# Kernel optimization log

Measured on AMD Instinct MI355X. Metric: run time of the kernel, lower is better.

Reference implementation:

```python
import jax, jax.numpy as jnp
import numpy as np

N_HEAD = 16
N_EMBD = 64  # per-head dim in this module's convention
INNER = N_HEAD * N_EMBD  # 1024


def setup_inputs() -> dict:
    key = jax.random.key(0)
    ks = jax.random.split(key, 6)
    B, S = 4, 2048
    scale = 0.02
    return {
        "x": jax.random.normal(ks[0], (B, S, N_EMBD), dtype=jnp.float32),
        "Wq": jax.random.normal(ks[1], (N_EMBD, INNER), dtype=jnp.float32) * scale,
        "Wk": jax.random.normal(ks[2], (N_EMBD, INNER), dtype=jnp.float32) * scale,
        "Wv": jax.random.normal(ks[3], (N_EMBD, INNER), dtype=jnp.float32) * scale,
        "Wo": jax.random.normal(ks[4], (INNER, N_EMBD), dtype=jnp.float32) * scale,
        "bo": jax.random.normal(ks[5], (N_EMBD,), dtype=jnp.float32) * scale,
        "causal_mask": 1,
    }


def reference(x, Wq, Wk, Wv, Wo, bo, causal_mask):
    B, S, _ = x.shape
    # projections: [B,S,INNER] -> [B,H,S,D]
    def split_heads(t):
        return t.reshape(B, S, N_HEAD, N_EMBD).transpose(0, 2, 1, 3)
    q = split_heads(x @ Wq)
    k = split_heads(x @ Wk)
    v = split_heads(x @ Wv)
    # [B,H,S,S]
    scores = jnp.einsum("bhqd,bhkd->bhqk", q, k) / jnp.sqrt(jnp.float32(N_EMBD))
    if causal_mask:
        future = jnp.triu(jnp.ones((S, S), dtype=scores.dtype), k=1)
        scores = scores - 1e9 * future  # matches torch: subtract 1e9*mask
    attn = jax.nn.softmax(scores, axis=-1)
    out = jnp.einsum("bhqk,bhkd->bhqd", attn, v)
    out = out.transpose(0, 2, 1, 3).reshape(B, S, INNER)
    return out @ Wo + bo
```

## Files before the change

kernel.cpp:

```cpp
#include <hip/hip_runtime.h>
#include <hip/hip_bf16.h>

#define NHEAD 16
#define HDIM 64
#define DINNER 1024
#define NBATCH 4
#define SEQ 2048
#define NTOK (NBATCH*SEQ)

typedef __bf16 bf16;
typedef __bf16 bf16x2 __attribute__((ext_vector_type(2)));
typedef __bf16 bf16x4 __attribute__((ext_vector_type(4)));
typedef __bf16 bf16x8 __attribute__((ext_vector_type(8)));
typedef float f32x4 __attribute__((ext_vector_type(4)));
typedef float f32x16 __attribute__((ext_vector_type(16)));
typedef unsigned int u32;
typedef unsigned int u32x2 __attribute__((ext_vector_type(2)));
typedef unsigned int u32x4 __attribute__((ext_vector_type(4)));

#define OFF_BO   8
#define OFF_XB   128
#define OFF_WQT  (OFF_XB + NTOK*HDIM)
#define OFF_WKT  (OFF_WQT + DINNER*HDIM)
#define OFF_WVT  (OFF_WKT + DINNER*HDIM)
#define OFF_WOT  (OFF_WVT + DINNER*HDIM)
#define OFF_Q    (OFF_WOT + DINNER*HDIM)
#define OFF_K    (OFF_Q + NTOK*DINNER)
#define OFF_VT   (OFF_K + NTOK*DINNER)
#define OFF_ATT  (OFF_VT + NTOK*DINNER)
#define OFF_ATT2 (OFF_ATT + NTOK*DINNER)
#define OFF_L    (OFF_ATT2 + NTOK*DINNER)

#define SSCALE 0.18033688011112042f

static __device__ __forceinline__ bf16x8 ld8(const bf16* p) {
  return *reinterpret_cast<const bf16x8*>(p);
}

static __device__ __forceinline__ u32 pkbf(float a, float b) {
  bf16x2 t; t[0] = (bf16)a; t[1] = (bf16)b;
  return __builtin_bit_cast(u32, t);
}

static __device__ __forceinline__ int detect_isbf(const void* x, int tid,
                                                  int* sflag) {
  if (tid < 64) {
    const unsigned short* xb = (const unsigned short*)x;
    bool ok = true;
#pragma unroll
    for (int i = 0; i < 8; i++) {
      unsigned e = (xb[tid * 8 + i] >> 7) & 0xFF;
      ok = ok && (e >= 64 && e <= 140);
    }
    unsigned long long mball = __ballot(ok);
    if (tid == 0) *sflag = (mball == ~0ull) ? 1 : 0;
  }
  __syncthreads();
  return *sflag;
}

__global__ __launch_bounds__(256) void prep_kernel(
    const void* __restrict__ x, const void* __restrict__ Wq,
    const void* __restrict__ Wk, const void* __restrict__ Wv,
    const void* __restrict__ Wo, const void* __restrict__ bo,
    bf16* __restrict__ ws) {
  __shared__ int sflag;
  int isbf = detect_isbf(x, threadIdx.x, &sflag);
  int z = blockIdx.y;
  int idx = blockIdx.x * 256 + threadIdx.x;
  if (z < 3) {
    const void* src = (z == 0) ? Wq : (z == 1) ? Wk : Wv;
    bf16* dst = ws + ((z == 0) ? OFF_WQT : (z == 1) ? OFF_WKT : OFF_WVT);
    int d = idx >> 10, n = idx & 1023;
    float v = isbf ? (float)((const bf16*)src)[idx] : ((const float*)src)[idx];
    if (z == 0) v *= SSCALE;
    dst[n * HDIM + d] = (bf16)v;
  } else if (z == 3) {
    int k = idx >> 6, n = idx & 63;
    float v = isbf ? (float)((const bf16*)Wo)[idx] : ((const float*)Wo)[idx];
    ws[OFF_WOT + n * DINNER + k] = (bf16)v;
  } else if (z == 4) {
    int i = idx * 8;
    bf16x8 v;
    if (isbf) {
      v = ld8((const bf16*)x + i);
    } else {
      f32x4 a = *reinterpret_cast<const f32x4*>((const float*)x + i);
      f32x4 b2 = *reinterpret_cast<const f32x4*>((const float*)x + i + 4);
#pragma unroll
      for (int j = 0; j < 4; j++) { v[j] = (bf16)a[j]; v[4 + j] = (bf16)b2[j]; }
    }
    *reinterpret_cast<bf16x8*>(&ws[OFF_XB + i]) = v;
  } else {
    if (idx < 64) ws[OFF_BO + idx] = isbf ? ((const bf16*)bo)[idx] : (bf16)((const float*)bo)[idx];
  }
}

__global__ __launch_bounds__(256) void qkv_kernel(bf16* __restrict__ ws) {
  __shared__ __align__(16) bf16 Vst[4][16 * 72];
  int tt = blockIdx.x, pz = blockIdx.z;
  int w = threadIdx.x >> 6;
  int nc = blockIdx.y * 4 + w;
  int lane = threadIdx.x & 63;
  int lq = lane & 15, quad = lane >> 4;
  const bf16* WT = ws + OFF_WQT + pz * (DINNER * HDIM);
  int n0 = nc * 64;
  bf16x8 w0[4], w1[4];
#pragma unroll
  for (int c = 0; c < 4; c++) {
    const bf16* wr = WT + (n0 + c * 16 + lq) * HDIM;
    w0[c] = ld8(wr + quad * 8);
    w1[c] = ld8(wr + 32 + quad * 8);
  }
  bf16* Qb = ws + OFF_Q;
  bf16* Kb = ws + OFF_K;
  bf16* VTb = ws + OFF_VT;
  bf16x8 ao0[4], ao1[4];
  if (pz == 2) {
    const bf16* WoT = ws + OFF_WOT;
#pragma unroll
    for (int c = 0; c < 4; c++) {
      const bf16* orow = WoT + (size_t)(c * 16 + lq) * DINNER + nc * 64;
      ao0[c] = ld8(orow + quad * 8);
      ao1[c] = ld8(orow + 32 + quad * 8);
    }
  }
#pragma unroll
  for (int mi = 0; mi < 4; mi++) {
    int t0 = tt * 64 + mi * 16;
    const bf16* xrow = ws + OFF_XB + (t0 + lq) * HDIM;
    bf16x8 x0 = ld8(xrow + quad * 8);
    bf16x8 x1 = ld8(xrow + 32 + quad * 8);
    int b = t0 >> 11, s0 = t0 & (SEQ - 1);
    if (pz < 2) {
#pragma unroll
      for (int c = 0; c < 4; c++) {
        f32x4 z = {0.f, 0.f, 0.f, 0.f};
        z = __builtin_amdgcn_mfma_f32_16x16x32_bf16(w0[c], x0, z, 0, 0, 0);
        z = __builtin_amdgcn_mfma_f32_16x16x32_bf16(w1[c], x1, z, 0, 0, 0);
        bf16x4 pk = {(bf16)z[0], (bf16)z[1], (bf16)z[2], (bf16)z[3]};
        bf16* P = (pz == 0) ? Qb : Kb;
        *reinterpret_cast<bf16x4*>(
            &P[((size_t)(b * NHEAD + nc) * SEQ + s0 + lq) * HDIM + c * 16 + quad * 4]) = pk;
      }
    } else {
#pragma unroll
      for (int c = 0; c < 4; c++) {
        f32x4 z = {0.f, 0.f, 0.f, 0.f};
        z = __builtin_amdgcn_mfma_f32_16x16x32_bf16(w0[c], x0, z, 0, 0, 0);
        z = __builtin_amdgcn_mfma_f32_16x16x32_bf16(w1[c], x1, z, 0, 0, 0);
        bf16x4 pk = {(bf16)z[0], (bf16)z[1], (bf16)z[2], (bf16)z[3]};
        *reinterpret_cast<bf16x4*>(&Vst[w][lq * 72 + c * 16 + quad * 4]) = pk;
      }
      bf16x8 bv0 = ld8(&Vst[w][lq * 72 + quad * 8]);
      bf16x8 bv1 = ld8(&Vst[w][lq * 72 + 32 + quad * 8]);
#pragma unroll
      for (int c = 0; c < 4; c++) {
        f32x4 z2 = {0.f, 0.f, 0.f, 0.f};
        z2 = __builtin_amdgcn_mfma_f32_16x16x32_bf16(ao0[c], bv0, z2, 0, 0, 0);
        z2 = __builtin_amdgcn_mfma_f32_16x16x32_bf16(ao1[c], bv1, z2, 0, 0, 0);
#pragma unroll
        for (int r = 0; r < 4; r++) {
          int d = c * 16 + quad * 4 + r;
          VTb[(((size_t)b * NHEAD + nc) * HDIM + d) * SEQ + s0 + lq] = (bf16)z2[r];
        }
      }
    }
  }
}

__global__ __launch_bounds__(256, 2) void flash_kernel(const int* __restrict__ cmask,
                                                       bf16* __restrict__ ws) {
  __shared__ __align__(16) bf16 Kl[2][64 * 64];
  __shared__ __align__(16) bf16 Vl[2][64 * 64];
  int bid = blockIdx.x;
  int bh = (bid & 7) * 8 + ((bid >> 3) & 7);
  int z = (bid >> 6) & 7;
  int half = bid >> 9;
  int w = threadIdx.x >> 6;
  int lane = threadIdx.x & 63;
  int ql = lane & 31, lh = lane >> 5, l7 = lane & 7;
  int causal = cmask[0];
  const bf16* Q = ws + OFF_Q + (size_t)bh * SEQ * HDIM;
  const bf16* K = ws + OFF_K + (size_t)bh * SEQ * HDIM;
  const bf16* VT = ws + OFF_VT + (size_t)bh * HDIM * SEQ;
  int b = bh >> 4, h = bh & 15;
  bf16* ar = ws + OFF_ATT + (size_t)half * NTOK * DINNER;
  float* Lp = reinterpret_cast<float*>(ws + OFF_L) + (size_t)half * NTOK * NHEAD;
  int sr = threadIdx.x >> 2;
  int sg = (threadIdx.x & 3) * 16;
  int sc0 = (((threadIdx.x & 3) * 2) ^ (sr & 7)) << 3;
  int sc1 = (((threadIdx.x & 3) * 2 + 1) ^ (sr & 7)) << 3;

  int bufc = 0;

  for (int seg = 0; seg < 2; ++seg) {
    int qt = seg ? (15 - z) : z;
    int Ts = causal ? (seg ? (32 - 2 * z) : (2 * z + 2)) : 32;
    int hs = Ts >> 1;
    int t0 = half * hs, t1 = t0 + hs;
    int qb = qt * 128;
    int qw = qb + w * 32;
    int qa = qw + ql;

    bf16x8 bq[4];
#pragma unroll
    for (int dsub = 0; dsub < 4; dsub++)
      bq[dsub] = ld8(Q + (size_t)qa * HDIM + dsub * 16 + lh * 8);

    f32x16 o0, o1;
#pragma unroll
    for (int r = 0; r < 16; r++) { o0[r] = 0.f; o1[r] = 0.f; }
    float lsum = 0.f;

    bf16x8 kst0 = ld8(K + (size_t)(t0 * 64 + sr) * HDIM + sg);
    bf16x8 kst1 = ld8(K + (size_t)(t0 * 64 + sr) * HDIM + sg + 8);
    bf16x8 vst0 = ld8(VT + (size_t)sr * SEQ + t0 * 64 + sg);
    bf16x8 vst1 = ld8(VT + (size_t)sr * SEQ + t0 * 64 + sg + 8);

    for (int ti = t0; ti < t1; ++ti, ++bufc) {
      int buf = bufc & 1;
      int k0 = ti * 64;
      *reinterpret_cast<bf16x8*>(&Kl[buf][sr * 64 + sc0]) = kst0;
      *reinterpret_cast<bf16x8*>(&Kl[buf][sr * 64 + sc1]) = kst1;
      *reinterpret_cast<bf16x8*>(&Vl[buf][sr * 64 + sc0]) = vst0;
      *reinterpret_cast<bf16x8*>(&Vl[buf][sr * 64 + sc1]) = vst1;
      int kn = (ti + 1 < t1) ? (k0 + 64) : k0;
      kst0 = ld8(K + (size_t)(kn + sr) * HDIM + sg);
      kst1 = ld8(K + (size_t)(kn + sr) * HDIM + sg + 8);
      vst0 = ld8(VT + (size_t)sr * SEQ + kn + sg);
      vst1 = ld8(VT + (size_t)sr * SEQ + kn + sg + 8);
      __syncthreads();
      if (causal && k0 > qw + 31) continue;

      f32x16 s0, s1;
#pragma unroll
      for (int r = 0; r < 16; r++) { s0[r] = 0.f; s1[r] = 0.f; }
      __builtin_amdgcn_s_setprio(1);
#pragma unroll
      for (int dsub = 0; dsub < 4; dsub++) {
        int co = ((dsub * 2 + lh) ^ l7) << 3;
        bf16x8 a0 = ld8(&Kl[buf][ql * 64 + co]);
        bf16x8 a1 = ld8(&Kl[buf][(32 + ql) * 64 + co]);
        s0 = __builtin_amdgcn_mfma_f32_32x32x16_bf16(a0, bq[dsub], s0, 0, 0, 0);
        s1 = __builtin_amdgcn_mfma_f32_32x32x16_bf16(a1, bq[dsub], s1, 0, 0, 0);
      }
      __builtin_amdgcn_s_setprio(0);

      if (causal && (k0 + 63 > qw)) {
#pragma unroll
        for (int r = 0; r < 16; r++) {
          int kk = k0 + (r & 3) + 8 * (r >> 2) + 4 * lh;
          if (kk > qa) s0[r] = -200.0f;
          if (kk + 32 > qa) s1[r] = -200.0f;
        }
      }

      bf16x8 pf[4];
      {
        float e[16];
#pragma unroll
        for (int r = 0; r < 16; r++) { e[r] = exp2f(s0[r]); lsum += e[r]; }
#pragma unroll
        for (int j = 0; j < 2; j++) {
          u32 x0 = pkbf(e[8 * j + 0], e[8 * j + 1]);
          u32 x1 = pkbf(e[8 * j + 2], e[8 * j + 3]);
          u32 y0 = pkbf(e[8 * j + 4], e[8 * j + 5]);
          u32 y1 = pkbf(e[8 * j + 6], e[8 * j + 7]);
          u32x2 r0 = __builtin_amdgcn_permlane32_swap(x0, y0, false, false);
          u32x2 r1 = __builtin_amdgcn_permlane32_swap(x1, y1, false, false);
          u32x4 fw = {r0[0], r1[0], r0[1], r1[1]};
          pf[j] = __builtin_bit_cast(bf16x8, fw);
        }
      }
      {
        float e[16];
#pragma unroll
        for (int r = 0; r < 16; r++) { e[r] = exp2f(s1[r]); lsum += e[r]; }
#pragma unroll
        for (int j = 0; j < 2; j++) {
          u32 x0 = pkbf(e[8 * j + 0], e[8 * j + 1]);
          u32 x1 = pkbf(e[8 * j + 2], e[8 * j + 3]);
          u32 y0 = pkbf(e[8 * j + 4], e[8 * j + 5]);
          u32 y1 = pkbf(e[8 * j + 6], e[8 * j + 7]);
          u32x2 r0 = __builtin_amdgcn_permlane32_swap(x0, y0, false, false);
          u32x2 r1 = __builtin_amdgcn_permlane32_swap(x1, y1, false, false);
          u32x4 fw = {r0[0], r1[0], r0[1], r1[1]};
          pf[2 + j] = __builtin_bit_cast(bf16x8, fw);
        }
      }

      __builtin_amdgcn_s_setprio(1);
#pragma unroll
      for (int ks = 0; ks < 4; ks++) {
        int co = ((ks * 2 + lh) ^ l7) << 3;
        bf16x8 av0 = ld8(&Vl[buf][ql * 64 + co]);
        bf16x8 av1 = ld8(&Vl[buf][(32 + ql) * 64 + co]);
        o0 = __builtin_amdgcn_mfma_f32_32x32x16_bf16(av0, pf[ks], o0, 0, 0, 0);
        o1 = __builtin_amdgcn_mfma_f32_32x32x16_bf16(av1, pf[ks], o1, 0, 0, 0);
      }
      __builtin_amdgcn_s_setprio(0);
    }

    lsum += __shfl_xor(lsum, 32);
    size_t row = (size_t)(b * SEQ) + qa;
    if (lane < 32) Lp[row * NHEAD + h] = lsum;
    size_t rowoff = row * DINNER + (size_t)h * HDIM;
#pragma unroll
    for (int g = 0; g < 4; g++) {
      bf16x4 ov0 = {(bf16)o0[4 * g], (bf16)o0[4 * g + 1],
                    (bf16)o0[4 * g + 2], (bf16)o0[4 * g + 3]};
      bf16x4 ov1 = {(bf16)o1[4 * g], (bf16)o1[4 * g + 1],
                    (bf16)o1[4 * g + 2], (bf16)o1[4 * g + 3]};
      *reinterpret_cast<bf16x4*>(&ar[rowoff + 8 * g + 4 * lh]) = ov0;
      *reinterpret_cast<bf16x4*>(&ar[rowoff + 32 + 8 * g + 4 * lh]) = ov1;
    }
  }
}

__global__ __launch_bounds__(256) void reduce_kernel(const bf16* __restrict__ ws,
                                                     const void* __restrict__ x,
                                                     void* __restrict__ outp) {
  __shared__ int sflag;
  int isbf = detect_isbf(x, threadIdx.x, &sflag);
  int idx = blockIdx.x * 256 + threadIdx.x;
  int t = idx >> 6, d = idx & 63;
  const bf16* a0 = ws + OFF_ATT + (size_t)t * DINNER + d;
  const bf16* a1 = a0 + (size_t)NTOK * DINNER;
  const float* l0 = reinterpret_cast<const float*>(ws + OFF_L) + (size_t)t * NHEAD;
  const float* l1 = l0 + (size_t)NTOK * NHEAD;
  float s = (float)ws[OFF_BO + d];
#pragma unroll
  for (int h = 0; h < 16; h++) {
    float inv = 1.0f / (l0[h] + l1[h]);
    s += ((float)a0[h * 64] + (float)a1[h * 64]) * inv;
  }
  if (isbf) ((bf16*)outp)[idx] = (bf16)s;
  else      ((float*)outp)[idx] = s;
}

extern "C" void kernel_launch(void* const* d_in, const int* in_sizes, int n_in,
                              void* d_out, int out_size, void* d_ws, size_t ws_size,
                              hipStream_t stream) {
  const void* x  = d_in[0];
  const void* Wq = d_in[1];
  const void* Wk = d_in[2];
  const void* Wv = d_in[3];
  const void* Wo = d_in[4];
  const void* bo = d_in[5];
  const int* cm  = (const int*)d_in[6];
  bf16* ws = (bf16*)d_ws;

  hipLaunchKernelGGL(prep_kernel, dim3(256, 6), dim3(256), 0, stream,
                     x, Wq, Wk, Wv, Wo, bo, ws);
  hipLaunchKernelGGL(qkv_kernel, dim3(128, 4, 3), dim3(256), 0, stream, ws);
  hipLaunchKernelGGL(flash_kernel, dim3(1024), dim3(256), 0, stream, cm, ws);
  hipLaunchKernelGGL(reduce_kernel, dim3(2048), dim3(256), 0, stream, ws, x, d_out);
}
```

Measured before the change: 170.3 us.

## Load K/V tiles directly from global memory into registers, drop LDS staging

Removes the double-buffered shared-memory staging of K and V tiles, along with the per-tile __syncthreads. Each wave now loads its MFMA operands for K and V^T straight from global memory. V loads are issued before the softmax so their latency can overlap the exp work. This removes LDS traffic and block-wide barriers, but every wave (4 per block) now fetches the same K/V tiles separately and relies on L1/L2 for reuse, with less coalesced 16-byte row accesses.

After: 237.7 us. 39.5% more time.

```diff
diff --git a/kernel.cpp b/kernel.cpp
--- a/kernel.cpp
+++ b/kernel.cpp
@@ -171,15 +171,13 @@
 
 __global__ __launch_bounds__(256, 2) void flash_kernel(const int* __restrict__ cmask,
                                                        bf16* __restrict__ ws) {
-  __shared__ __align__(16) bf16 Kl[2][64 * 64];
-  __shared__ __align__(16) bf16 Vl[2][64 * 64];
   int bid = blockIdx.x;
   int bh = (bid & 7) * 8 + ((bid >> 3) & 7);
   int z = (bid >> 6) & 7;
   int half = bid >> 9;
   int w = threadIdx.x >> 6;
   int lane = threadIdx.x & 63;
-  int ql = lane & 31, lh = lane >> 5, l7 = lane & 7;
+  int ql = lane & 31, lh = lane >> 5;
   int causal = cmask[0];
   const bf16* Q = ws + OFF_Q + (size_t)bh * SEQ * HDIM;
   const bf16* K = ws + OFF_K + (size_t)bh * SEQ * HDIM;
@@ -187,12 +185,6 @@
   int b = bh >> 4, h = bh & 15;
   bf16* ar = ws + OFF_ATT + (size_t)half * NTOK * DINNER;
   float* Lp = reinterpret_cast<float*>(ws + OFF_L) + (size_t)half * NTOK * NHEAD;
-  int sr = threadIdx.x >> 2;
-  int sg = (threadIdx.x & 3) * 16;
-  int sc0 = (((threadIdx.x & 3) * 2) ^ (sr & 7)) << 3;
-  int sc1 = (((threadIdx.x & 3) * 2 + 1) ^ (sr & 7)) << 3;
-
-  int bufc = 0;
 
   for (int seg = 0; seg < 2; ++seg) {
     int qt = seg ? (15 - z) : z;
@@ -213,24 +205,8 @@
     for (int r = 0; r < 16; r++) { o0[r] = 0.f; o1[r] = 0.f; }
     float lsum = 0.f;
 
-    bf16x8 kst0 = ld8(K + (size_t)(t0 * 64 + sr) * HDIM + sg);
-    bf16x8 kst1 = ld8(K + (size_t)(t0 * 64 + sr) * HDIM + sg + 8);
-    bf16x8 vst0 = ld8(VT + (size_t)sr * SEQ + t0 * 64 + sg);
-    bf16x8 vst1 = ld8(VT + (size_t)sr * SEQ + t0 * 64 + sg + 8);
-
-    for (int ti = t0; ti < t1; ++ti, ++bufc) {
-      int buf = bufc & 1;
+    for (int ti = t0; ti < t1; ++ti) {
       int k0 = ti * 64;
-      *reinterpret_cast<bf16x8*>(&Kl[buf][sr * 64 + sc0]) = kst0;
-      *reinterpret_cast<bf16x8*>(&Kl[buf][sr * 64 + sc1]) = kst1;
-      *reinterpret_cast<bf16x8*>(&Vl[buf][sr * 64 + sc0]) = vst0;
-      *reinterpret_cast<bf16x8*>(&Vl[buf][sr * 64 + sc1]) = vst1;
-      int kn = (ti + 1 < t1) ? (k0 + 64) : k0;
-      kst0 = ld8(K + (size_t)(kn + sr) * HDIM + sg);
-      kst1 = ld8(K + (size_t)(kn + sr) * HDIM + sg + 8);
-      vst0 = ld8(VT + (size_t)sr * SEQ + kn + sg);
-      vst1 = ld8(VT + (size_t)sr * SEQ + kn + sg + 8);
-      __syncthreads();
       if (causal && k0 > qw + 31) continue;
 
       f32x16 s0, s1;
@@ -239,13 +215,19 @@
       __builtin_amdgcn_s_setprio(1);
 #pragma unroll
       for (int dsub = 0; dsub < 4; dsub++) {
-        int co = ((dsub * 2 + lh) ^ l7) << 3;
-        bf16x8 a0 = ld8(&Kl[buf][ql * 64 + co]);
-        bf16x8 a1 = ld8(&Kl[buf][(32 + ql) * 64 + co]);
+        bf16x8 a0 = ld8(K + (size_t)(k0 + ql) * HDIM + dsub * 16 + lh * 8);
+        bf16x8 a1 = ld8(K + (size_t)(k0 + 32 + ql) * HDIM + dsub * 16 + lh * 8);
         s0 = __builtin_amdgcn_mfma_f32_32x32x16_bf16(a0, bq[dsub], s0, 0, 0, 0);
         s1 = __builtin_amdgcn_mfma_f32_32x32x16_bf16(a1, bq[dsub], s1, 0, 0, 0);
       }
       __builtin_amdgcn_s_setprio(0);
+
+      bf16x8 av0[4], av1[4];
+#pragma unroll
+      for (int ks = 0; ks < 4; ks++) {
+        av0[ks] = ld8(VT + (size_t)ql * SEQ + k0 + ks * 16 + lh * 8);
+        av1[ks] = ld8(VT + (size_t)(32 + ql) * SEQ + k0 + ks * 16 + lh * 8);
+      }
 
       if (causal && (k0 + 63 > qw)) {
 #pragma unroll
@@ -293,11 +275,8 @@
       __builtin_amdgcn_s_setprio(1);
 #pragma unroll
       for (int ks = 0; ks < 4; ks++) {
-        int co = ((ks * 2 + lh) ^ l7) << 3;
-        bf16x8 av0 = ld8(&Vl[buf][ql * 64 + co]);
-        bf16x8 av1 = ld8(&Vl[buf][(32 + ql) * 64 + co]);
-        o0 = __builtin_amdgcn_mfma_f32_32x32x16_bf16(av0, pf[ks], o0, 0, 0, 0);
-        o1 = __builtin_amdgcn_mfma_f32_32x32x16_bf16(av1, pf[ks], o1, 0, 0, 0);
+        o0 = __builtin_amdgcn_mfma_f32_32x32x16_bf16(av0[ks], pf[ks], o0, 0, 0, 0);
+        o1 = __builtin_amdgcn_mfma_f32_32x32x16_bf16(av1[ks], pf[ks], o1, 0, 0, 0);
       }
       __builtin_amdgcn_s_setprio(0);
     }
```

## Drop split-KV flash halves, normalize in-kernel via MFMA row sums, coalesce prep transposes

Applied to the files above, without the earlier changes.

The flash kernel no longer splits each query tile's key range into two halves with partial outputs and L sums that are merged later. Each block now handles one query tile over its whole causal range, using a static map to interleave long and short tiles. The row sum is computed by an extra MFMA against a ones vector, and outputs are normalized before the store, so the reduce kernel only sums heads plus bias. The prep kernel's weight transposes now go through shared-memory tiles for coalesced access, and the V transpose store is vectorized by swapping the MFMA operands. This halves the attention intermediate traffic, at the cost of longer per-block critical paths, possible load imbalance, and one extra MFMA per K tile.

Measured after the change: 173.3 us. About the same (+1.7%).

```diff
diff --git a/kernel.cpp b/kernel.cpp
--- a/kernel.cpp
+++ b/kernel.cpp
@@ -28,8 +28,6 @@
 #define OFF_K    (OFF_Q + NTOK*DINNER)
 #define OFF_VT   (OFF_K + NTOK*DINNER)
 #define OFF_ATT  (OFF_VT + NTOK*DINNER)
-#define OFF_ATT2 (OFF_ATT + NTOK*DINNER)
-#define OFF_L    (OFF_ATT2 + NTOK*DINNER)
 
 #define SSCALE 0.18033688011112042f
 
@@ -64,22 +62,50 @@
     const void* __restrict__ Wk, const void* __restrict__ Wv,
     const void* __restrict__ Wo, const void* __restrict__ bo,
     bf16* __restrict__ ws) {
+  __shared__ __align__(16) bf16 T[64][80];
   __shared__ int sflag;
-  int isbf = detect_isbf(x, threadIdx.x, &sflag);
   int z = blockIdx.y;
-  int idx = blockIdx.x * 256 + threadIdx.x;
+  int bx = blockIdx.x;
+  int tid = threadIdx.x;
+  if (z < 4 && bx >= 16) return;
+  int isbf = detect_isbf(x, tid, &sflag);
   if (z < 3) {
     const void* src = (z == 0) ? Wq : (z == 1) ? Wk : Wv;
     bf16* dst = ws + ((z == 0) ? OFF_WQT : (z == 1) ? OFF_WKT : OFF_WVT);
-    int d = idx >> 10, n = idx & 1023;
-    float v = isbf ? (float)((const bf16*)src)[idx] : ((const float*)src)[idx];
-    if (z == 0) v *= SSCALE;
-    dst[n * HDIM + d] = (bf16)v;
+#pragma unroll
+    for (int p = 0; p < 16; p++) {
+      int i2 = p * 256 + tid;
+      int d = i2 >> 6, nl = i2 & 63;
+      int gi = d * 1024 + bx * 64 + nl;
+      float v = isbf ? (float)((const bf16*)src)[gi] : ((const float*)src)[gi];
+      if (z == 0) v *= SSCALE;
+      T[nl][d] = (bf16)v;
+    }
+    __syncthreads();
+#pragma unroll
+    for (int p = 0; p < 2; p++) {
+      int nl = p * 32 + (tid >> 3), d8 = (tid & 7) * 8;
+      bf16x8 v = ld8(&T[nl][d8]);
+      *reinterpret_cast<bf16x8*>(&dst[(bx * 64 + nl) * 64 + d8]) = v;
+    }
   } else if (z == 3) {
-    int k = idx >> 6, n = idx & 63;
-    float v = isbf ? (float)((const bf16*)Wo)[idx] : ((const float*)Wo)[idx];
-    ws[OFF_WOT + n * DINNER + k] = (bf16)v;
+#pragma unroll
+    for (int p = 0; p < 16; p++) {
+      int i2 = p * 256 + tid;
+      int kk = i2 >> 6, n = i2 & 63;
+      int gi = (bx * 64 + kk) * 64 + n;
+      float v = isbf ? (float)((const bf16*)Wo)[gi] : ((const float*)Wo)[gi];
+      T[n][kk] = (bf16)v;
+    }
+    __syncthreads();
+#pragma unroll
+    for (int p = 0; p < 2; p++) {
+      int n = p * 32 + (tid >> 3), k8 = (tid & 7) * 8;
+      bf16x8 v = ld8(&T[n][k8]);
+      *reinterpret_cast<bf16x8*>(&ws[OFF_WOT + n * DINNER + bx * 64 + k8]) = v;
+    }
   } else if (z == 4) {
+    int idx = bx * 256 + tid;
     int i = idx * 8;
     bf16x8 v;
     if (isbf) {
@@ -92,6 +118,7 @@
     }
     *reinterpret_cast<bf16x8*>(&ws[OFF_XB + i]) = v;
   } else {
+    int idx = bx * 256 + tid;
     if (idx < 64) ws[OFF_BO + idx] = isbf ? ((const bf16*)bo)[idx] : (bf16)((const float*)bo)[idx];
   }
 }
@@ -157,13 +184,11 @@
 #pragma unroll
       for (int c = 0; c < 4; c++) {
         f32x4 z2 = {0.f, 0.f, 0.f, 0.f};
-        z2 = __builtin_amdgcn_mfma_f32_16x16x32_bf16(ao0[c], bv0, z2, 0, 0, 0);
-        z2 = __builtin_amdgcn_mfma_f32_16x16x32_bf16(ao1[c], bv1, z2, 0, 0, 0);
-#pragma unroll
-        for (int r = 0; r < 4; r++) {
-          int d = c * 16 + quad * 4 + r;
-          VTb[(((size_t)b * NHEAD + nc) * HDIM + d) * SEQ + s0 + lq] = (bf16)z2[r];
-        }
+        z2 = __builtin_amdgcn_mfma_f32_16x16x32_bf16(bv0, ao0[c], z2, 0, 0, 0);
+        z2 = __builtin_amdgcn_mfma_f32_16x16x32_bf16(bv1, ao1[c], z2, 0, 0, 0);
+        bf16x4 pk = {(bf16)z2[0], (bf16)z2[1], (bf16)z2[2], (bf16)z2[3]};
+        *reinterpret_cast<bf16x4*>(
+            &VTb[(((size_t)b * NHEAD + nc) * HDIM + c * 16 + lq) * SEQ + s0 + quad * 4]) = pk;
       }
     }
   }
@@ -173,10 +198,10 @@
                                                        bf16* __restrict__ ws) {
   __shared__ __align__(16) bf16 Kl[2][64 * 64];
   __shared__ __align__(16) bf16 Vl[2][64 * 64];
+  const int qmap[16] = {15,13,11,9,0,2,4,6,14,12,10,8,1,3,5,7};
   int bid = blockIdx.x;
   int bh = (bid & 7) * 8 + ((bid >> 3) & 7);
-  int z = (bid >> 6) & 7;
-  int half = bid >> 9;
+  int qt = qmap[bid >> 6];
   int w = threadIdx.x >> 6;
   int lane = threadIdx.x & 63;
   int ql = lane & 31, lh = lane >> 5, l7 = lane & 7;
@@ -185,136 +210,130 @@
   const bf16* K = ws + OFF_K + (size_t)bh * SEQ * HDIM;
   const bf16* VT = ws + OFF_VT + (size_t)bh * HDIM * SEQ;
   int b = bh >> 4, h = bh & 15;
-  bf16* ar = ws + OFF_ATT + (size_t)half * NTOK * DINNER;
-  float* Lp = reinterpret_cast<float*>(ws + OFF_L) + (size_t)half * NTOK * NHEAD;
+  bf16* ar = ws + OFF_ATT;
   int sr = threadIdx.x >> 2;
   int sg = (threadIdx.x & 3) * 16;
   int sc0 = (((threadIdx.x & 3) * 2) ^ (sr & 7)) << 3;
   int sc1 = (((threadIdx.x & 3) * 2 + 1) ^ (sr & 7)) << 3;
 
-  int bufc = 0;
-
-  for (int seg = 0; seg < 2; ++seg) {
-    int qt = seg ? (15 - z) : z;
-    int Ts = causal ? (seg ? (32 - 2 * z) : (2 * z + 2)) : 32;
-    int hs = Ts >> 1;
-    int t0 = half * hs, t1 = t0 + hs;
-    int qb = qt * 128;
-    int qw = qb + w * 32;
-    int qa = qw + ql;
-
-    bf16x8 bq[4];
-#pragma unroll
-    for (int dsub = 0; dsub < 4; dsub++)
-      bq[dsub] = ld8(Q + (size_t)qa * HDIM + dsub * 16 + lh * 8);
-
-    f32x16 o0, o1;
-#pragma unroll
-    for (int r = 0; r < 16; r++) { o0[r] = 0.f; o1[r] = 0.f; }
-    float lsum = 0.f;
-
-    bf16x8 kst0 = ld8(K + (size_t)(t0 * 64 + sr) * HDIM + sg);
-    bf16x8 kst1 = ld8(K + (size_t)(t0 * 64 + sr) * HDIM + sg + 8);
-    bf16x8 vst0 = ld8(VT + (size_t)sr * SEQ + t0 * 64 + sg);
-    bf16x8 vst1 = ld8(VT + (size_t)sr * SEQ + t0 * 64 + sg + 8);
-
-    for (int ti = t0; ti < t1; ++ti, ++bufc) {
-      int buf = bufc & 1;
-      int k0 = ti * 64;
-      *reinterpret_cast<bf16x8*>(&Kl[buf][sr * 64 + sc0]) = kst0;
-      *reinterpret_cast<bf16x8*>(&Kl[buf][sr * 64 + sc1]) = kst1;
-      *reinterpret_cast<bf16x8*>(&Vl[buf][sr * 64 + sc0]) = vst0;
-      *reinterpret_cast<bf16x8*>(&Vl[buf][sr * 64 + sc1]) = vst1;
-      int kn = (ti + 1 < t1) ? (k0 + 64) : k0;
-      kst0 = ld8(K + (size_t)(kn + sr) * HDIM + sg);
-      kst1 = ld8(K + (size_t)(kn + sr) * HDIM + sg + 8);
-      vst0 = ld8(VT + (size_t)sr * SEQ + kn + sg);
-      vst1 = ld8(VT + (size_t)sr * SEQ + kn + sg + 8);
-      __syncthreads();
-      if (causal && k0 > qw + 31) continue;
-
-      f32x16 s0, s1;
-#pragma unroll
-      for (int r = 0; r < 16; r++) { s0[r] = 0.f; s1[r] = 0.f; }
-      __builtin_amdgcn_s_setprio(1);
-#pragma unroll
-      for (int dsub = 0; dsub < 4; dsub++) {
-        int co = ((dsub * 2 + lh) ^ l7) << 3;
-        bf16x8 a0 = ld8(&Kl[buf][ql * 64 + co]);
-        bf16x8 a1 = ld8(&Kl[buf][(32 + ql) * 64 + co]);
-        s0 = __builtin_amdgcn_mfma_f32_32x32x16_bf16(a0, bq[dsub], s0, 0, 0, 0);
-        s1 = __builtin_amdgcn_mfma_f32_32x32x16_bf16(a1, bq[dsub], s1, 0, 0, 0);
-      }
-      __builtin_amdgcn_s_setprio(0);
-
-      if (causal && (k0 + 63 > qw)) {
-#pragma unroll
-        for (int r = 0; r < 16; r++) {
-          int kk = k0 + (r & 3) + 8 * (r >> 2) + 4 * lh;
-          if (kk > qa) s0[r] = -200.0f;
-          if (kk + 32 > qa) s1[r] = -200.0f;
-        }
-      }
-
-      bf16x8 pf[4];
-      {
-        float e[16];
-#pragma unroll
-        for (int r = 0; r < 16; r++) { e[r] = exp2f(s0[r]); lsum += e[r]; }
-#pragma unroll
-        for (int j = 0; j < 2; j++) {
-          u32 x0 = pkbf(e[8 * j + 0], e[8 * j + 1]);
-          u32 x1 = pkbf(e[8 * j + 2], e[8 * j + 3]);
-          u32 y0 = pkbf(e[8 * j + 4], e[8 * j + 5]);
-          u32 y1 = pkbf(e[8 * j + 6], e[8 * j + 7]);
-          u32x2 r0 = __builtin_amdgcn_permlane32_swap(x0, y0, false, false);
-          u32x2 r1 = __builtin_amdgcn_permlane32_swap(x1, y1, false, false);
-          u32x4 fw = {r0[0], r1[0], r0[1], r1[1]};
-          pf[j] = __builtin_bit_cast(bf16x8, fw);
-        }
-      }
-      {
-        float e[16];
-#pragma unroll
-        for (int r = 0; r < 16; r++) { e[r] = exp2f(s1[r]); lsum += e[r]; }
-#pragma unroll
-        for (int j = 0; j < 2; j++) {
-          u32 x0 = pkbf(e[8 * j + 0], e[8 * j + 1]);
-          u32 x1 = pkbf(e[8 * j + 2], e[8 * j + 3]);
-          u32 y0 = pkbf(e[8 * j + 4], e[8 * j + 5]);
-          u32 y1 = pkbf(e[8 * j + 6], e[8 * j + 7]);
-          u32x2 r0 = __builtin_amdgcn_permlane32_swap(x0, y0, false, false);
-          u32x2 r1 = __builtin_amdgcn_permlane32_swap(x1, y1, false, false);
-          u32x4 fw = {r0[0], r1[0], r0[1], r1[1]};
-          pf[2 + j] = __builtin_bit_cast(bf16x8, fw);
-        }
-      }
-
-      __builtin_amdgcn_s_setprio(1);
-#pragma unroll
-      for (int ks = 0; ks < 4; ks++) {
-        int co = ((ks * 2 + lh) ^ l7) << 3;
-        bf16x8 av0 = ld8(&Vl[buf][ql * 64 + co]);
-        bf16x8 av1 = ld8(&Vl[buf][(32 + ql) * 64 + co]);
-        o0 = __builtin_amdgcn_mfma_f32_32x32x16_bf16(av0, pf[ks], o0, 0, 0, 0);
-        o1 = __builtin_amdgcn_mfma_f32_32x32x16_bf16(av1, pf[ks], o1, 0, 0, 0);
-      }
-      __builtin_amdgcn_s_setprio(0);
-    }
-
-    lsum += __shfl_xor(lsum, 32);
-    size_t row = (size_t)(b * SEQ) + qa;
-    if (lane < 32) Lp[row * NHEAD + h] = lsum;
-    size_t rowoff = row * DINNER + (size_t)h * HDIM;
-#pragma unroll
-    for (int g = 0; g < 4; g++) {
-      bf16x4 ov0 = {(bf16)o0[4 * g], (bf16)o0[4 * g + 1],
-                    (bf16)o0[4 * g + 2], (bf16)o0[4 * g + 3]};
-      bf16x4 ov1 = {(bf16)o1[4 * g], (bf16)o1[4 * g + 1],
-                    (bf16)o1[4 * g + 2], (bf16)o1[4 * g + 3]};
-      *reinterpret_cast<bf16x4*>(&ar[rowoff + 8 * g + 4 * lh]) = ov0;
-      *reinterpret_cast<bf16x4*>(&ar[rowoff + 32 + 8 * g + 4 * lh]) = ov1;
-    }
+  int qb = qt * 128;
+  int qw = qb + w * 32;
+  int qa = qw + ql;
+  int T = (causal ? (qb + 128) : SEQ) / 64;
+
+  bf16x8 af1;
+#pragma unroll
+  for (int j = 0; j < 8; j++) af1[j] = (bf16)1.0f;
+
+  bf16x8 bq[4];
+#pragma unroll
+  for (int dsub = 0; dsub < 4; dsub++)
+    bq[dsub] = ld8(Q + (size_t)qa * HDIM + dsub * 16 + lh * 8);
+
+  f32x16 o0, o1, la;
+#pragma unroll
+  for (int r = 0; r < 16; r++) { o0[r] = 0.f; o1[r] = 0.f; la[r] = 0.f; }
+
+  bf16x8 kst0 = ld8(K + (size_t)sr * HDIM + sg);
+  bf16x8 kst1 = ld8(K + (size_t)sr * HDIM + sg + 8);
+  bf16x8 vst0 = ld8(VT + (size_t)sr * SEQ + sg);
+  bf16x8 vst1 = ld8(VT + (size_t)sr * SEQ + sg + 8);
+
+  for (int ti = 0; ti < T; ++ti) {
+    int buf = ti & 1;
+    int k0 = ti * 64;
+    *reinterpret_cast<bf16x8*>(&Kl[buf][sr * 64 + sc0]) = kst0;
+    *reinterpret_cast<bf16x8*>(&Kl[buf][sr * 64 + sc1]) = kst1;
+    *reinterpret_cast<bf16x8*>(&Vl[buf][sr * 64 + sc0]) = vst0;
+    *reinterpret_cast<bf16x8*>(&Vl[buf][sr * 64 + sc1]) = vst1;
+    int kn = (ti + 1 < T) ? (k0 + 64) : k0;
+    kst0 = ld8(K + (size_t)(kn + sr) * HDIM + sg);
+    kst1 = ld8(K + (size_t)(kn + sr) * HDIM + sg + 8);
+    vst0 = ld8(VT + (size_t)sr * SEQ + kn + sg);
+    vst1 = ld8(VT + (size_t)sr * SEQ + kn + sg + 8);
+    __syncthreads();
+    if (causal && k0 > qw + 31) continue;
+
+    f32x16 s0, s1;
+#pragma unroll
+    for (int r = 0; r < 16; r++) { s0[r] = 0.f; s1[r] = 0.f; }
+    __builtin_amdgcn_s_setprio(1);
+#pragma unroll
+    for (int dsub = 0; dsub < 4; dsub++) {
+      int co = ((dsub * 2 + lh) ^ l7) << 3;
+      bf16x8 a0 = ld8(&Kl[buf][ql * 64 + co]);
+      bf16x8 a1 = ld8(&Kl[buf][(32 + ql) * 64 + co]);
+      s0 = __builtin_amdgcn_mfma_f32_32x32x16_bf16(a0, bq[dsub], s0, 0, 0, 0);
+      s1 = __builtin_amdgcn_mfma_f32_32x32x16_bf16(a1, bq[dsub], s1, 0, 0, 0);
+    }
+    __builtin_amdgcn_s_setprio(0);
+
+    if (causal && (k0 + 63 > qw)) {
+#pragma unroll
+      for (int r = 0; r < 16; r++) {
+        int kk = k0 + (r & 3) + 8 * (r >> 2) + 4 * lh;
+        if (kk > qa) s0[r] = -200.0f;
+        if (kk + 32 > qa) s1[r] = -200.0f;
+      }
+    }
+
+    bf16x8 pf[4];
+    {
+      float e[16];
+#pragma unroll
+      for (int r = 0; r < 16; r++) e[r] = exp2f(s0[r]);
+#pragma unroll
+      for (int j = 0; j < 2; j++) {
+        u32 x0 = pkbf(e[8 * j + 0], e[8 * j + 1]);
+        u32 x1 = pkbf(e[8 * j + 2], e[8 * j + 3]);
+        u32 y0 = pkbf(e[8 * j + 4], e[8 * j + 5]);
+        u32 y1 = pkbf(e[8 * j + 6], e[8 * j + 7]);
+        u32x2 r0 = __builtin_amdgcn_permlane32_swap(x0, y0, false, false);
+        u32x2 r1 = __builtin_amdgcn_permlane32_swap(x1, y1, false, false);
+        u32x4 fw = {r0[0], r1[0], r0[1], r1[1]};
+        pf[j] = __builtin_bit_cast(bf16x8, fw);
+      }
+    }
+    {
+      float e[16];
+#pragma unroll
+      for (int r = 0; r < 16; r++) e[r] = exp2f(s1[r]);
+#pragma unroll
+      for (int j = 0; j < 2; j++) {
+        u32 x0 = pkbf(e[8 * j + 0], e[8 * j + 1]);
+        u32 x1 = pkbf(e[8 * j + 2], e[8 * j + 3]);
+        u32 y0 = pkbf(e[8 * j + 4], e[8 * j + 5]);
+        u32 y1 = pkbf(e[8 * j + 6], e[8 * j + 7]);
+        u32x2 r0 = __builtin_amdgcn_permlane32_swap(x0, y0, false, false);
+        u32x2 r1 = __builtin_amdgcn_permlane32_swap(x1, y1, false, false);
+        u32x4 fw = {r0[0], r1[0], r0[1], r1[1]};
+        pf[2 + j] = __builtin_bit_cast(bf16x8, fw);
+      }
+    }
+
+    __builtin_amdgcn_s_setprio(1);
+#pragma unroll
+    for (int ks = 0; ks < 4; ks++) {
+      int co = ((ks * 2 + lh) ^ l7) << 3;
+      bf16x8 av0 = ld8(&Vl[buf][ql * 64 + co]);
+      bf16x8 av1 = ld8(&Vl[buf][(32 + ql) * 64 + co]);
+      o0 = __builtin_amdgcn_mfma_f32_32x32x16_bf16(av0, pf[ks], o0, 0, 0, 0);
+      o1 = __builtin_amdgcn_mfma_f32_32x32x16_bf16(av1, pf[ks], o1, 0, 0, 0);
+      la = __builtin_amdgcn_mfma_f32_32x32x16_bf16(af1, pf[ks], la, 0, 0, 0);
+    }
+    __builtin_amdgcn_s_setprio(0);
+  }
+
+  float inv = 1.0f / la[0];
+  size_t rowoff = ((size_t)(b * SEQ) + qa) * DINNER + (size_t)h * HDIM;
+#pragma unroll
+  for (int g = 0; g < 4; g++) {
+    bf16x4 ov0 = {(bf16)(o0[4 * g] * inv), (bf16)(o0[4 * g + 1] * inv),
+                  (bf16)(o0[4 * g + 2] * inv), (bf16)(o0[4 * g + 3] * inv)};
+    bf16x4 ov1 = {(bf16)(o1[4 * g] * inv), (bf16)(o1[4 * g + 1] * inv),
+                  (bf16)(o1[4 * g + 2] * inv), (bf16)(o1[4 * g + 3] * inv)};
+    *reinterpret_cast<bf16x4*>(&ar[rowoff + 8 * g + 4 * lh]) = ov0;
+    *reinterpret_cast<bf16x4*>(&ar[rowoff + 32 + 8 * g + 4 * lh]) = ov1;
   }
 }
 
@@ -325,16 +344,10 @@
   int isbf = detect_isbf(x, threadIdx.x, &sflag);
   int idx = blockIdx.x * 256 + threadIdx.x;
   int t = idx >> 6, d = idx & 63;
-  const bf16* a0 = ws + OFF_ATT + (size_t)t * DINNER + d;
-  const bf16* a1 = a0 + (size_t)NTOK * DINNER;
-  const float* l0 = reinterpret_cast<const float*>(ws + OFF_L) + (size_t)t * NHEAD;
-  const float* l1 = l0 + (size_t)NTOK * NHEAD;
+  const bf16* ar = ws + OFF_ATT + (size_t)t * DINNER + d;
   float s = (float)ws[OFF_BO + d];
 #pragma unroll
-  for (int h = 0; h < 16; h++) {
-    float inv = 1.0f / (l0[h] + l1[h]);
-    s += ((float)a0[h * 64] + (float)a1[h * 64]) * inv;
-  }
+  for (int h = 0; h < 16; h++) s += (float)ar[h * 64];
   if (isbf) ((bf16*)outp)[idx] = (bf16)s;
   else      ((float*)outp)[idx] = s;
 }
```
